# Kernel tuning notes

Measured on AMD Instinct MI355X. Metric: run time of the kernel, lower is better.

Reference implementation:

```python
import jax, jax.numpy as jnp
import numpy as np

N_HEAD = 16

def setup_inputs() -> dict:
    key = jax.random.key(0)
    k1, k2, k3 = jax.random.split(key, 3)
    B, K, C = 2, 2048, 1024
    x = jax.random.normal(k1, (B, K, C), dtype=jnp.float32)
    W_qkv = jax.random.normal(k2, (C, 3 * C), dtype=jnp.float32) * (1.0 / np.sqrt(C))
    b_qkv = jnp.zeros((3 * C,), dtype=jnp.float32)
    W_proj = jax.random.normal(k3, (C, C), dtype=jnp.float32) * (1.0 / np.sqrt(C))
    b_proj = jnp.zeros((C,), dtype=jnp.float32)
    return {"x": x, "W_qkv": W_qkv, "b_qkv": b_qkv, "W_proj": W_proj, "b_proj": b_proj, "K": K}

def reference(x, W_qkv, b_qkv, W_proj, b_proj, K):
    B, _, C = x.shape
    H = N_HEAD
    Dh = C // H
    qkv = x @ W_qkv + b_qkv                      # [B, K, 3C]
    q, k, v = jnp.split(qkv, 3, axis=-1)
    # [B, H, K, Dh]
    q = q.reshape(B, K, H, Dh).transpose(0, 2, 1, 3)
    k = k.reshape(B, K, H, Dh).transpose(0, 2, 1, 3)
    v = v.reshape(B, K, H, Dh).transpose(0, 2, 1, 3)
    att = jnp.einsum('bhqd,bhkd->bhqk', q, k) / jnp.sqrt(jnp.asarray(Dh, dtype=x.dtype))
    causal = jnp.tril(jnp.ones((K, K), dtype=bool))
    att = jnp.where(causal[None, None], att, jnp.asarray(-jnp.inf, dtype=x.dtype))
    att = jax.nn.softmax(att, axis=-1)
    y = jnp.einsum('bhqk,bhkd->bhqd', att, v)    # [B, H, K, Dh]
    y = y.transpose(0, 2, 1, 3).reshape(B, K, C)
    return y @ W_proj + b_proj
```

## Files before the change

kernel.cpp:

```cpp
#include <hip/hip_runtime.h>
#include <hip/hip_bf16.h>
#include <math.h>

typedef __attribute__((ext_vector_type(8))) short short8;
typedef __attribute__((ext_vector_type(4))) float f32x4;
typedef __attribute__((ext_vector_type(4))) short short4v;
typedef __attribute__((ext_vector_type(2))) int int2v;

static __device__ __forceinline__ short f2bf(float f) {
    __hip_bfloat16 h = __float2bfloat16(f);
    return *reinterpret_cast<short*>(&h);
}
static __device__ __forceinline__ void store_out(float* p, float v) { *p = v; }
static __device__ __forceinline__ void store_out(short* p, float v) { *p = f2bf(v); }

#define GLL16(g, l) __builtin_amdgcn_global_load_lds( \
    (const __attribute__((address_space(1))) void*)(g), \
    (__attribute__((address_space(3))) void*)(l), 16, 0, 0)

#if __has_builtin(__builtin_amdgcn_exp2f)
#define EXP2(x) __builtin_amdgcn_exp2f(x)
#else
#define EXP2(x) exp2f(x)
#endif

#if __has_builtin(__builtin_amdgcn_cvt_pk_bf16_f32)
typedef __attribute__((ext_vector_type(2))) __bf16 bf16x2;
static __device__ __forceinline__ int pack2bf(float a, float b) {
    bf16x2 r = __builtin_amdgcn_cvt_pk_bf16_f32(a, b);
    return __builtin_bit_cast(int, r);
}
#else
static __device__ __forceinline__ int pack2bf(float a, float b) {
    unsigned ua = __builtin_bit_cast(unsigned, a) + 0x8000u;
    unsigned ub = __builtin_bit_cast(unsigned, b) + 0x8000u;
    return (int)((ua >> 16) | (ub & 0xFFFF0000u));
}
#endif

static __device__ __forceinline__ void transpose_cast_tile(
    const float* __restrict__ W, short* __restrict__ Wt, int Kd, int N,
    int bx, int by)
{
    __shared__ float ts[32][33];
    const int c0 = bx * 32, r0 = by * 32;
    const int tx = threadIdx.x & 31, ty = threadIdx.x >> 5;
    #pragma unroll
    for (int e = 0; e < 4; ++e)
        ts[ty + e * 8][tx] = W[(size_t)(r0 + ty + e * 8) * N + c0 + tx];
    __syncthreads();
    #pragma unroll
    for (int e = 0; e < 4; ++e)
        Wt[(size_t)(c0 + ty + e * 8) * Kd + r0 + tx] = f2bf(ts[tx][ty + e * 8]);
}

__global__ __launch_bounds__(256) void prep_kernel(
    const float* __restrict__ x,      short* __restrict__ xb,    int nx,
    const float* __restrict__ W_qkv,  short* __restrict__ Wt1,
    const float* __restrict__ W_proj, short* __restrict__ Wt2,
    int C)
{
    const int nbx = nx / 1024;
    const int nb1 = (3 * C / 32) * (C / 32);
    int bid = blockIdx.x;
    if (bid < nbx) {
        int i = (bid * 256 + threadIdx.x) * 4;
        float4 v = *(const float4*)(x + i);
        short4v o = { f2bf(v.x), f2bf(v.y), f2bf(v.z), f2bf(v.w) };
        *(short4v*)(xb + i) = o;
        return;
    }
    bid -= nbx;
    if (bid < nb1) {
        const int nc = 3 * C / 32;
        transpose_cast_tile(W_qkv, Wt1, C, 3 * C, bid % nc, bid / nc);
        return;
    }
    bid -= nb1;
    {
        const int nc = C / 32;
        transpose_cast_tile(W_proj, Wt2, C, C, bid % nc, bid / nc);
    }
}

#define GK 32

__global__ __launch_bounds__(256) void gemm_qkv_kernel(
    const short* __restrict__ A, const short* __restrict__ Bt,
    const float* __restrict__ bias,
    short* __restrict__ qb, short* __restrict__ kvp,
    int M, int N, int Kd, int C, int Ktok, float qscale)
{
    __shared__ __attribute__((aligned(16))) short smem[17408];
    short* As = smem;
    short* Bs = smem + 4096;
    short* T  = smem;

    const int tid  = threadIdx.x;
    const int lane = tid & 63, w = tid >> 6;
    const int col  = lane & 15, quad = lane >> 4;
    const int wm = (w & 1) * 64, wn = (w >> 1) * 64;

    const int nwg  = gridDim.x * gridDim.y;
    const int bid0 = blockIdx.y * gridDim.x + blockIdx.x;
    const int bid  = (bid0 & 7) * (nwg >> 3) + (bid0 >> 3);
    const int row0 = (bid / gridDim.x) * 128, col0 = (bid % gridDim.x) * 128;

    const int sr = tid >> 2, scg = (tid & 3) * 8;
    const short* gA = A  + (size_t)(row0 + sr) * Kd + scg;
    const short* gB = Bt + (size_t)(col0 + sr) * Kd + scg;
    short* lA = As + sr * GK + scg;
    short* lB = Bs + sr * GK + scg;
    const size_t skip = (size_t)64 * Kd;

    f32x4 acc[4][4] = {};
    for (int k0 = 0; k0 < Kd; k0 += GK) {
        __syncthreads();
        GLL16(gA,        lA);
        GLL16(gA + skip, lA + 64 * GK);
        GLL16(gB,        lB);
        GLL16(gB + skip, lB + 64 * GK);
        gA += GK; gB += GK;
        __syncthreads();

        short8 aF[4], bF[4];
        #pragma unroll
        for (int mt = 0; mt < 4; ++mt)
            aF[mt] = *(const short8*)&As[(wm + mt * 16 + col) * GK + quad * 8];
        #pragma unroll
        for (int nt = 0; nt < 4; ++nt)
            bF[nt] = *(const short8*)&Bs[(wn + nt * 16 + col) * GK + quad * 8];
        #pragma unroll
        for (int mt = 0; mt < 4; ++mt)
            #pragma unroll
            for (int nt = 0; nt < 4; ++nt)
                acc[mt][nt] = __builtin_amdgcn_mfma_f32_16x16x32_bf16(aF[mt], bF[nt], acc[mt][nt], 0, 0, 0);
    }

    if (col0 < C) {
        #pragma unroll
        for (int mt = 0; mt < 4; ++mt)
            #pragma unroll
            for (int i = 0; i < 4; ++i) {
                const size_t r = row0 + wm + mt * 16 + quad * 4 + i;
                #pragma unroll
                for (int nt = 0; nt < 4; ++nt) {
                    const int c = col0 + wn + nt * 16 + col;
                    qb[r * C + c] = f2bf((acc[mt][nt][i] + bias[c]) * qscale);
                }
            }
        return;
    }

    const bool isK = col0 < 2 * C;
    __syncthreads();
    #pragma unroll
    for (int mt = 0; mt < 4; ++mt) {
        const int rr0 = wm + mt * 16 + quad * 4;
        #pragma unroll
        for (int nt = 0; nt < 4; ++nt) {
            const int cr = wn + nt * 16 + col;
            const float bb_ = bias[col0 + cr];
            if (isK) {
                #pragma unroll
                for (int i = 0; i < 4; ++i)
                    T[(rr0 + i) * 136 + cr] = f2bf(acc[mt][nt][i] + bb_);
            } else {
                short4v pk = { f2bf(acc[mt][nt][0] + bb_),
                               f2bf(acc[mt][nt][1] + bb_),
                               f2bf(acc[mt][nt][2] + bb_),
                               f2bf(acc[mt][nt][3] + bb_) };
                *(short4v*)&T[cr * 136 + rr0] = pk;
            }
        }
    }
    __syncthreads();

    const int bb  = row0 / Ktok, k0t = row0 % Ktok;
    const int h0  = (col0 - (isK ? C : 2 * C)) >> 6;
    #pragma unroll
    for (int j = 0; j < 8; ++j) {
        const int s     = tid + j * 256;
        const int lane2 = s & 63, f = (s >> 6) & 3, cil = (s >> 8) & 3, hl = s >> 10;
        const int col2  = lane2 & 15, quad2 = lane2 >> 4;
        short8 d;
        if (isK) {
            const int nb = f >> 1, half = f & 1;
            d = *(const short8*)&T[(cil * 32 + 2 * col2 + nb) * 136
                                   + hl * 64 + half * 32 + quad2 * 8];
        } else {
            d = *(const short8*)&T[(hl * 64 + f * 16 + col2) * 136
                                   + cil * 32 + quad2 * 8];
        }
        const int bh = bb * 16 + h0 + hl;
        const int ci = (k0t >> 5) + cil;
        const int fr = isK ? f : 4 + f;
        *(short8*)(kvp + (((size_t)bh * 64 + ci) * 8 + fr) * 512 + lane2 * 8) = d;
    }
}

template <typename OutT, int GM, int GN>
__global__ __launch_bounds__(256) void gemm_mfma_kernel(
    const short* __restrict__ A, const short* __restrict__ Bt,
    const float* __restrict__ bias, OutT* __restrict__ C,
    int M, int N, int Kd)
{
    constexpr int WM = GM / 2, WN = GN / 2;
    __shared__ __attribute__((aligned(16))) short As[GM * GK];
    __shared__ __attribute__((aligned(16))) short Bs[GN * GK];
    const int tid  = threadIdx.x;
    const int lane = tid & 63, w = tid >> 6;
    const int col  = lane & 15, quad = lane >> 4;
    const int wm = (w & 1) * WM, wn = (w >> 1) * WN;

    const int nwg  = gridDim.x * gridDim.y;
    const int bid0 = blockIdx.y * gridDim.x + blockIdx.x;
    const int bid  = (bid0 & 7) * (nwg >> 3) + (bid0 >> 3);
    const int row0 = (bid / gridDim.x) * GM, col0 = (bid % gridDim.x) * GN;

    const int sr = tid >> 2, scg = (tid & 3) * 8;
    const short* gA = A  + (size_t)(row0 + sr) * Kd + scg;
    const short* gB = Bt + (size_t)(col0 + sr) * Kd + scg;
    short* lA = As + sr * GK + scg;
    short* lB = Bs + sr * GK + scg;
    const size_t skip = (size_t)64 * Kd;

    f32x4 acc[WM / 16][WN / 16] = {};
    for (int k0 = 0; k0 < Kd; k0 += GK) {
        __syncthreads();
        #pragma unroll
        for (int t = 0; t < GM / 64; ++t) GLL16(gA + t * skip, lA + t * 64 * GK);
        #pragma unroll
        for (int t = 0; t < GN / 64; ++t) GLL16(gB + t * skip, lB + t * 64 * GK);
        gA += GK; gB += GK;
        __syncthreads();

        short8 aF[WM / 16], bF[WN / 16];
        #pragma unroll
        for (int mt = 0; mt < WM / 16; ++mt)
            aF[mt] = *(const short8*)&As[(wm + mt * 16 + col) * GK + quad * 8];
        #pragma unroll
        for (int nt = 0; nt < WN / 16; ++nt)
            bF[nt] = *(const short8*)&Bs[(wn + nt * 16 + col) * GK + quad * 8];
        #pragma unroll
        for (int mt = 0; mt < WM / 16; ++mt)
            #pragma unroll
            for (int nt = 0; nt < WN / 16; ++nt)
                acc[mt][nt] = __builtin_amdgcn_mfma_f32_16x16x32_bf16(aF[mt], bF[nt], acc[mt][nt], 0, 0, 0);
    }

    #pragma unroll
    for (int mt = 0; mt < WM / 16; ++mt)
        #pragma unroll
        for (int i = 0; i < 4; ++i) {
            const size_t r = row0 + wm + mt * 16 + quad * 4 + i;
            #pragma unroll
            for (int nt = 0; nt < WN / 16; ++nt) {
                const int c = col0 + wn + nt * 16 + col;
                store_out(&C[r * N + c], acc[mt][nt][i] + bias[c]);
            }
        }
}

#define DH 64

__global__ __launch_bounds__(256, 4) void flash_mfma_kernel(
    const short* __restrict__ qb,
    const short* __restrict__ kvp,
    short* __restrict__ y,
    int K, int C)
{
    __shared__ __attribute__((aligned(16))) short smem[8704];

    const int tid  = threadIdx.x;
    const int lane = tid & 63, w = tid >> 6;
    const int col  = lane & 15, quad = lane >> 4;

    short* Pw = smem + w * 1280;

    const int cmb = blockIdx.x & 31;
    const int g   = blockIdx.x >> 5;
    const int b   = cmb >> 4, h = cmb & 15;

    short8 bOnes;
    #pragma unroll
    for (int j = 0; j < 8; ++j) bOnes[j] = (col == 0) ? (short)0x3F80 : (short)0;

    const short* qbase  = qb + (size_t)b * K * C + h * DH;
    const short* kvbase = kvp + (size_t)cmb * 64 * 4096 + lane * 8;

    struct Frag { short8 k[2][2]; short8 v[4]; };
    auto loadF = [&](Frag& f, int ci) {
        const short* p = kvbase + (size_t)ci * 4096;
        f.k[0][0] = *(const short8*)(p);
        f.k[0][1] = *(const short8*)(p + 512);
        f.k[1][0] = *(const short8*)(p + 1024);
        f.k[1][1] = *(const short8*)(p + 1536);
        f.v[0]    = *(const short8*)(p + 2048);
        f.v[1]    = *(const short8*)(p + 2560);
        f.v[2]    = *(const short8*)(p + 3072);
        f.v[3]    = *(const short8*)(p + 3584);
    };

    auto run = [&](int T) {
        const int t0 = T * 32;
        const int NC = T + 1;

        short8 aQ[2][2];
        #pragma unroll
        for (int qg = 0; qg < 2; ++qg) {
            const short* qp = qbase + (size_t)(t0 + qg * 16 + col) * C;
            aQ[qg][0] = *(const short8*)(qp + quad * 8);
            aQ[qg][1] = *(const short8*)(qp + 32 + quad * 8);
        }
        f32x4 O[2][4] = {};
        f32x4 L4[2] = {};

        for (int ci = w; ci < NC; ci += 4) {
            Frag f;
            loadF(f, ci);
            const int kc = ci * 32;
            __builtin_amdgcn_s_setprio(1);
            #pragma unroll
            for (int qg = 0; qg < 2; ++qg) {
                const int qb2 = t0 + qg * 16;
                short* Ptq = Pw + qg * 640;
                f32x4 S[2] = {};
                #pragma unroll
                for (int nb = 0; nb < 2; ++nb) {
                    S[nb] = __builtin_amdgcn_mfma_f32_16x16x32_bf16(aQ[qg][0], f.k[nb][0], S[nb], 0, 0, 0);
                    S[nb] = __builtin_amdgcn_mfma_f32_16x16x32_bf16(aQ[qg][1], f.k[nb][1], S[nb], 0, 0, 0);
                }
                if (kc + 31 <= qb2) {
                    #pragma unroll
                    for (int i = 0; i < 4; ++i)
                        *(int*)&Ptq[(quad * 4 + i) * 40 + col * 2] =
                            pack2bf(EXP2(S[0][i]), EXP2(S[1][i]));
                } else {
                    const int kg = kc + col * 2;
                    #pragma unroll
                    for (int i = 0; i < 4; ++i) {
                        const int q = qb2 + quad * 4 + i;
                        float s0 = (kg + 0 <= q) ? S[0][i] : -INFINITY;
                        float s1 = (kg + 1 <= q) ? S[1][i] : -INFINITY;
                        *(int*)&Ptq[(quad * 4 + i) * 40 + col * 2] =
                            pack2bf(EXP2(s0), EXP2(s1));
                    }
                }
                short8 aP = *(const short8*)&Ptq[col * 40 + quad * 8];
                #pragma unroll
                for (int db = 0; db < 4; ++db)
                    O[qg][db] = __builtin_amdgcn_mfma_f32_16x16x32_bf16(aP, f.v[db], O[qg][db], 0, 0, 0);
                L4[qg] = __builtin_amdgcn_mfma_f32_16x16x32_bf16(aP, bOnes, L4[qg], 0, 0, 0);
            }
            __builtin_amdgcn_s_setprio(0);
        }

        float* OrA = (float*)smem;
        float* OrB = OrA + 32 * 68;
        __syncthreads();
        if (w < 2) {
            float* R = (w == 0) ? OrA : OrB;
            #pragma unroll
            for (int qg = 0; qg < 2; ++qg)
                #pragma unroll
                for (int i = 0; i < 4; ++i) {
                    const int row = qg * 16 + quad * 4 + i;
                    #pragma unroll
                    for (int db = 0; db < 4; ++db)
                        R[row * 68 + db * 16 + col] = O[qg][db][i];
                    if (col == 0) R[row * 68 + 64] = L4[qg][i];
                }
        }
        __syncthreads();
        if (w >= 2) {
            float* R = (w == 2) ? OrA : OrB;
            #pragma unroll
            for (int qg = 0; qg < 2; ++qg)
                #pragma unroll
                for (int i = 0; i < 4; ++i) {
                    const int row = qg * 16 + quad * 4 + i;
                    #pragma unroll
                    for (int db = 0; db < 4; ++db)
                        R[row * 68 + db * 16 + col] += O[qg][db][i];
                    if (col == 0) R[row * 68 + 64] += L4[qg][i];
                }
        }
        __syncthreads();

        #pragma unroll
        for (int rstep = 0; rstep < 2; ++rstep) {
            const int row = w * 8 + rstep * 4 + quad;
            f32x4 oa = *(const f32x4*)&OrA[row * 68 + col * 4];
            f32x4 ob = *(const f32x4*)&OrB[row * 68 + col * 4];
            const float inv = 1.f / (OrA[row * 68 + 64] + OrB[row * 68 + 64]);
            int2v o2 = { pack2bf((oa[0] + ob[0]) * inv, (oa[1] + ob[1]) * inv),
                         pack2bf((oa[2] + ob[2]) * inv, (oa[3] + ob[3]) * inv) };
            *(int2v*)(y + ((size_t)b * K + t0 + row) * C + h * DH + col * 4) = o2;
        }
        __syncthreads();
    };

    run(g);
    run(63 - g);
}

extern "C" void kernel_launch(void* const* d_in, const int* in_sizes, int n_in,
                              void* d_out, int out_size, void* d_ws, size_t ws_size,
                              hipStream_t stream)
{
    const float* x      = (const float*)d_in[0];
    const float* W_qkv  = (const float*)d_in[1];
    const float* b_qkv  = (const float*)d_in[2];
    const float* W_proj = (const float*)d_in[3];
    const float* b_proj = (const float*)d_in[4];

    const int B = 2, K = 2048, C = 1024, H = 16;
    const int M = B * K;
    const float C2 = 0.18033688f;

    char* ws = (char*)d_ws;
    short* xb    = (short*)ws;  ws += (size_t)M * C * 2;
    short* Wt1   = (short*)ws;  ws += (size_t)3 * C * C * 2;
    short* Wt2   = (short*)ws;  ws += (size_t)C * C * 2;
    short* qb    = (short*)ws;  ws += (size_t)M * C * 2;
    short* yb    = (short*)ws;  ws += (size_t)M * C * 2;
    short* kvp   = (short*)ws;

    const int nbx = (M * C) / 1024;
    const int nb1 = (3 * C / 32) * (C / 32);
    const int nb2 = (C / 32) * (C / 32);
    prep_kernel<<<nbx + nb1 + nb2, 256, 0, stream>>>(x, xb, M * C, W_qkv, Wt1, W_proj, Wt2, C);

    dim3 g1((3 * C) / 128, M / 128);
    gemm_qkv_kernel<<<g1, 256, 0, stream>>>(xb, Wt1, b_qkv, qb, kvp, M, 3 * C, C, C, K, C2);

    flash_mfma_kernel<<<dim3(32 * 32), 256, 0, stream>>>(qb, kvp, yb, K, C);

    dim3 g3(C / 64, M / 128);
    gemm_mfma_kernel<float, 128, 64><<<g3, 256, 0, stream>>>(yb, Wt2, b_proj, (float*)d_out, M, C, C);
}
```

Baseline: 171.6 us.

## Double GEMM K-tile to 64 with XOR-swizzled LDS layout

```diff
diff --git a/kernel.cpp b/kernel.cpp
--- a/kernel.cpp
+++ b/kernel.cpp
@@ -83,7 +83,7 @@
     }
 }
 
-#define GK 32
+#define GK 64
 
 __global__ __launch_bounds__(256) void gemm_qkv_kernel(
     const short* __restrict__ A, const short* __restrict__ Bt,
@@ -93,7 +93,7 @@
 {
     __shared__ __attribute__((aligned(16))) short smem[17408];
     short* As = smem;
-    short* Bs = smem + 4096;
+    short* Bs = smem + 8192;
     short* T  = smem;
 
     const int tid  = threadIdx.x;
@@ -106,35 +106,41 @@
     const int bid  = (bid0 & 7) * (nwg >> 3) + (bid0 >> 3);
     const int row0 = (bid / gridDim.x) * 128, col0 = (bid % gridDim.x) * 128;
 
-    const int sr = tid >> 2, scg = (tid & 3) * 8;
-    const short* gA = A  + (size_t)(row0 + sr) * Kd + scg;
-    const short* gB = Bt + (size_t)(col0 + sr) * Kd + scg;
-    short* lA = As + sr * GK + scg;
-    short* lB = Bs + sr * GK + scg;
-    const size_t skip = (size_t)64 * Kd;
+    const int sr  = tid >> 3;
+    const int sxg = ((tid & 7) ^ (sr & 7)) * 8;
+    const short* gA = A  + (size_t)(row0 + sr) * Kd + sxg;
+    const short* gB = Bt + (size_t)(col0 + sr) * Kd + sxg;
+    short* lA = As + tid * 8;
+    short* lB = Bs + tid * 8;
+    const size_t skip32 = (size_t)32 * Kd;
 
     f32x4 acc[4][4] = {};
     for (int k0 = 0; k0 < Kd; k0 += GK) {
         __syncthreads();
-        GLL16(gA,        lA);
-        GLL16(gA + skip, lA + 64 * GK);
-        GLL16(gB,        lB);
-        GLL16(gB + skip, lB + 64 * GK);
+        #pragma unroll
+        for (int t = 0; t < 4; ++t) GLL16(gA + t * skip32, lA + t * 2048);
+        #pragma unroll
+        for (int t = 0; t < 4; ++t) GLL16(gB + t * skip32, lB + t * 2048);
         gA += GK; gB += GK;
         __syncthreads();
 
-        short8 aF[4], bF[4];
-        #pragma unroll
-        for (int mt = 0; mt < 4; ++mt)
-            aF[mt] = *(const short8*)&As[(wm + mt * 16 + col) * GK + quad * 8];
-        #pragma unroll
-        for (int nt = 0; nt < 4; ++nt)
-            bF[nt] = *(const short8*)&Bs[(wn + nt * 16 + col) * GK + quad * 8];
-        #pragma unroll
-        for (int mt = 0; mt < 4; ++mt)
+        #pragma unroll
+        for (int kk = 0; kk < 2; ++kk) {
+            short8 aF[4], bF[4];
+            #pragma unroll
+            for (int mt = 0; mt < 4; ++mt)
+                aF[mt] = *(const short8*)&As[(wm + mt * 16 + col) * 64
+                                             + (((kk * 4 + quad) ^ (col & 7)) * 8)];
             #pragma unroll
             for (int nt = 0; nt < 4; ++nt)
-                acc[mt][nt] = __builtin_amdgcn_mfma_f32_16x16x32_bf16(aF[mt], bF[nt], acc[mt][nt], 0, 0, 0);
+                bF[nt] = *(const short8*)&Bs[(wn + nt * 16 + col) * 64
+                                             + (((kk * 4 + quad) ^ (col & 7)) * 8)];
+            #pragma unroll
+            for (int mt = 0; mt < 4; ++mt)
+                #pragma unroll
+                for (int nt = 0; nt < 4; ++nt)
+                    acc[mt][nt] = __builtin_amdgcn_mfma_f32_16x16x32_bf16(aF[mt], bF[nt], acc[mt][nt], 0, 0, 0);
+        }
     }
 
     if (col0 < C) {
@@ -218,35 +224,41 @@
     const int bid  = (bid0 & 7) * (nwg >> 3) + (bid0 >> 3);
     const int row0 = (bid / gridDim.x) * GM, col0 = (bid % gridDim.x) * GN;
 
-    const int sr = tid >> 2, scg = (tid & 3) * 8;
-    const short* gA = A  + (size_t)(row0 + sr) * Kd + scg;
-    const short* gB = Bt + (size_t)(col0 + sr) * Kd + scg;
-    short* lA = As + sr * GK + scg;
-    short* lB = Bs + sr * GK + scg;
-    const size_t skip = (size_t)64 * Kd;
+    const int sr  = tid >> 3;
+    const int sxg = ((tid & 7) ^ (sr & 7)) * 8;
+    const short* gA = A  + (size_t)(row0 + sr) * Kd + sxg;
+    const short* gB = Bt + (size_t)(col0 + sr) * Kd + sxg;
+    short* lA = As + tid * 8;
+    short* lB = Bs + tid * 8;
+    const size_t skip32 = (size_t)32 * Kd;
 
     f32x4 acc[WM / 16][WN / 16] = {};
     for (int k0 = 0; k0 < Kd; k0 += GK) {
         __syncthreads();
         #pragma unroll
-        for (int t = 0; t < GM / 64; ++t) GLL16(gA + t * skip, lA + t * 64 * GK);
-        #pragma unroll
-        for (int t = 0; t < GN / 64; ++t) GLL16(gB + t * skip, lB + t * 64 * GK);
+        for (int t = 0; t < GM / 32; ++t) GLL16(gA + t * skip32, lA + t * 2048);
+        #pragma unroll
+        for (int t = 0; t < GN / 32; ++t) GLL16(gB + t * skip32, lB + t * 2048);
         gA += GK; gB += GK;
         __syncthreads();
 
-        short8 aF[WM / 16], bF[WN / 16];
-        #pragma unroll
-        for (int mt = 0; mt < WM / 16; ++mt)
-            aF[mt] = *(const short8*)&As[(wm + mt * 16 + col) * GK + quad * 8];
-        #pragma unroll
-        for (int nt = 0; nt < WN / 16; ++nt)
-            bF[nt] = *(const short8*)&Bs[(wn + nt * 16 + col) * GK + quad * 8];
-        #pragma unroll
-        for (int mt = 0; mt < WM / 16; ++mt)
+        #pragma unroll
+        for (int kk = 0; kk < 2; ++kk) {
+            short8 aF[WM / 16], bF[WN / 16];
+            #pragma unroll
+            for (int mt = 0; mt < WM / 16; ++mt)
+                aF[mt] = *(const short8*)&As[(wm + mt * 16 + col) * 64
+                                             + (((kk * 4 + quad) ^ (col & 7)) * 8)];
             #pragma unroll
             for (int nt = 0; nt < WN / 16; ++nt)
-                acc[mt][nt] = __builtin_amdgcn_mfma_f32_16x16x32_bf16(aF[mt], bF[nt], acc[mt][nt], 0, 0, 0);
+                bF[nt] = *(const short8*)&Bs[(wn + nt * 16 + col) * 64
+                                             + (((kk * 4 + quad) ^ (col & 7)) * 8)];
+            #pragma unroll
+            for (int mt = 0; mt < WM / 16; ++mt)
+                #pragma unroll
+                for (int nt = 0; nt < WN / 16; ++nt)
+                    acc[mt][nt] = __builtin_amdgcn_mfma_f32_16x16x32_bf16(aF[mt], bF[nt], acc[mt][nt], 0, 0, 0);
+        }
     }
 
     #pragma unroll
```

New measurement: 175.6 us. 1.02x slower.
